# Performance work log

Hardware: AMD Instinct MI355X
Metric: run time of the kernel (lower is better)

## Reference

```python
import jax, jax.numpy as jnp
import numpy as np

ALPHA = 0.1   # alpha_factor
BETA = 1.0    # beta_factor
NUM_CLASSES = 1000
B, D = 4096, 512


def setup_inputs() -> dict:
    key = jax.random.key(0)
    ks = jax.random.split(key, 7)
    return {
        "anchor": jax.random.normal(ks[0], (B, D), dtype=jnp.float32),
        "positive": jax.random.normal(ks[1], (B, D), dtype=jnp.float32),
        "negative": jax.random.normal(ks[2], (B, D), dtype=jnp.float32),
        "outputs": jax.random.normal(ks[3], (3 * B, NUM_CLASSES), dtype=jnp.float32),
        "labels_anchor": jax.random.randint(ks[4], (B,), 0, NUM_CLASSES, dtype=jnp.int32).astype(jnp.int64),
        "labels_neg": jax.random.randint(ks[5], (B,), 0, NUM_CLASSES, dtype=jnp.int32).astype(jnp.int64),
        "exemplars": jax.random.normal(ks[6], (NUM_CLASSES, D), dtype=jnp.float32),
    }


def reference(anchor, positive, negative, outputs, labels_anchor, labels_neg, exemplars):
    # cross-entropy (mean reduction) over concatenated labels [3B]
    labels = jnp.concatenate([labels_anchor, labels_anchor, labels_neg], axis=0)
    logp = jax.nn.log_softmax(outputs, axis=-1)                       # [3B, C]
    loss_softmax = -jnp.mean(jnp.take_along_axis(logp, labels[:, None], axis=1))

    # pairwise L2 distances anchor-to-exemplars via ||a||^2 + ||e||^2 - 2 a.e  -> [B, C]
    a_sq = jnp.sum(anchor * anchor, axis=1, keepdims=True)            # [B, 1]
    e_sq = jnp.sum(exemplars * exemplars, axis=1)[None, :]            # [1, C]
    d2 = a_sq + e_sq - 2.0 * (anchor @ exemplars.T)                   # [B, C]
    d_all = jnp.sqrt(jnp.maximum(d2, 0.0))

    d_ref = jnp.take_along_axis(d_all, labels_anchor[:, None], axis=1)[:, 0]  # [B]
    d_closest = jnp.min(d_all, axis=1)                                # [B]
    loss_center = jnp.sum(jax.nn.relu(d_ref - d_closest))

    tp = jnp.linalg.norm(anchor - positive, axis=1)                   # [B]
    tn = jnp.linalg.norm(anchor - negative, axis=1)                   # [B]
    loss_triplet = jnp.sum(jax.nn.relu(tp - tn))

    loss_total = loss_softmax + ALPHA * loss_center + BETA * loss_triplet
    return (loss_total, loss_triplet, loss_softmax, loss_center)
```

## Files before the change

### kernel.cpp

```cpp
#include <hip/hip_runtime.h>
#include <math.h>

#define BB 4096
#define DD 512
#define CC 1000

typedef __attribute__((ext_vector_type(8))) short short8;
typedef __attribute__((ext_vector_type(4))) float f32x4;

#define OFF_PMINP 0
#define OFF_DREF  32768
#define OFF_CEP   36864
#define OFF_TRP   38400

__device__ __forceinline__ unsigned short f2bf(float x) {
    unsigned u = __float_as_uint(x);
    unsigned r = (u + 0x7FFFu + ((u >> 16) & 1u)) >> 16;
    return (unsigned short)r;
}

__device__ __forceinline__ short8 cvt8(const float4 x, const float4 y, float& sq) {
    union { unsigned short u[8]; short8 v; } o;
    o.u[0]=f2bf(x.x); o.u[1]=f2bf(x.y); o.u[2]=f2bf(x.z); o.u[3]=f2bf(x.w);
    o.u[4]=f2bf(y.x); o.u[5]=f2bf(y.y); o.u[6]=f2bf(y.z); o.u[7]=f2bf(y.w);
    sq += x.x*x.x + x.y*x.y + x.z*x.z + x.w*x.w
        + y.x*y.x + y.y*y.y + y.z*y.z + y.w*y.w;
    return o.v;
}

__global__ __launch_bounds__(512) void main_kernel(
    const float* __restrict__ a, const float* __restrict__ p,
    const float* __restrict__ n, const float* __restrict__ ex,
    const float* __restrict__ outp,
    const int* __restrict__ la, const int* __restrict__ ln,
    float* __restrict__ pminp, float* __restrict__ ce_part,
    float* __restrict__ tr_part, float* __restrict__ dref)
{
    __shared__ unsigned short lA[128 * 64];
    __shared__ unsigned short lB[128 * 64];
    __shared__ float s_pm[4][128];
    __shared__ float s_aq[128], s_eq[128];
    __shared__ float ps[8];

    const int bid = blockIdx.x;
    const int tid = threadIdx.x;
    const int w = tid >> 6, lane = tid & 63;

    if (bid < 256) {
        const int strip = bid & 31, panel = bid >> 5;
        const int gm0 = strip * 128, gn0 = panel * 128;
        const int wm = w >> 2, wn = w & 3;
        const int hi = lane >> 4, lo = lane & 15;

        const int r0 = tid >> 3, s0 = tid & 7;
        const int g0 = s0 ^ (r0 & 7);
        const float4* srcA0 = (const float4*)(a + (size_t)(gm0 + r0) * DD) + (g0 << 1);
        const float4* srcA1 = (const float4*)(a + (size_t)(gm0 + 64 + r0) * DD) + (g0 << 1);
        const int er0 = gn0 + r0,      er0c = er0 < CC ? er0 : CC - 1;
        const int er1 = gn0 + 64 + r0, er1c = er1 < CC ? er1 : CC - 1;
        const float4* srcB0 = (const float4*)(ex + (size_t)er0c * DD) + (g0 << 1);
        const float4* srcB1 = (const float4*)(ex + (size_t)er1c * DD) + (g0 << 1);

        float4 a0, a0b, a1, a1b, b0, b0b, b1, b1b;
#define GLOAD(kt) do { \
        a0 = srcA0[(kt)*16]; a0b = srcA0[(kt)*16 + 1]; \
        a1 = srcA1[(kt)*16]; a1b = srcA1[(kt)*16 + 1]; \
        b0 = srcB0[(kt)*16]; b0b = srcB0[(kt)*16 + 1]; \
        b1 = srcB1[(kt)*16]; b1b = srcB1[(kt)*16 + 1]; \
    } while (0)

        float sa0 = 0.f, sa1 = 0.f, se0 = 0.f, se1 = 0.f;
        f32x4 acc[4][2];
#pragma unroll
        for (int mi = 0; mi < 4; mi++)
#pragma unroll
            for (int ni = 0; ni < 2; ni++) acc[mi][ni] = (f32x4){0.f, 0.f, 0.f, 0.f};

        GLOAD(0);
        for (int kt = 0; kt < 8; kt++) {
            *(short8*)&lA[tid << 3]         = cvt8(a0, a0b, sa0);
            *(short8*)&lA[(tid + 512) << 3] = cvt8(a1, a1b, sa1);
            *(short8*)&lB[tid << 3]         = cvt8(b0, b0b, se0);
            *(short8*)&lB[(tid + 512) << 3] = cvt8(b1, b1b, se1);
            __syncthreads();
            if (kt < 7) GLOAD(kt + 1);

#pragma unroll
            for (int kk = 0; kk < 2; kk++) {
                short8 af[4], bf[2];
#pragma unroll
                for (int mi = 0; mi < 4; mi++) {
                    int r = (wm << 6) + (mi << 4) + lo, s = (kk << 2) + hi;
                    af[mi] = *(const short8*)&lA[(r << 6) + ((s ^ (r & 7)) << 3)];
                }
#pragma unroll
                for (int ni = 0; ni < 2; ni++) {
                    int r = (wn << 5) + (ni << 4) + lo, s = (kk << 2) + hi;
                    bf[ni] = *(const short8*)&lB[(r << 6) + ((s ^ (r & 7)) << 3)];
                }
#pragma unroll
                for (int mi = 0; mi < 4; mi++)
#pragma unroll
                    for (int ni = 0; ni < 2; ni++)
                        acc[mi][ni] = __builtin_amdgcn_mfma_f32_16x16x32_bf16(af[mi], bf[ni], acc[mi][ni], 0, 0, 0);
            }
            __syncthreads();
        }
#undef GLOAD

#pragma unroll
        for (int off = 1; off < 8; off <<= 1) {
            sa0 += __shfl_xor(sa0, off);
            sa1 += __shfl_xor(sa1, off);
            se0 += __shfl_xor(se0, off);
            se1 += __shfl_xor(se1, off);
        }
        if ((lane & 7) == 0) {
            s_aq[r0] = sa0; s_aq[64 + r0] = sa1;
            s_eq[r0] = se0; s_eq[64 + r0] = se1;
        }
        __syncthreads();

        float aq[4][4];
#pragma unroll
        for (int mi = 0; mi < 4; mi++)
#pragma unroll
            for (int j = 0; j < 4; j++)
                aq[mi][j] = s_aq[wm * 64 + mi * 16 + hi * 4 + j];
        float esqc[2]; int bad[2];
#pragma unroll
        for (int ni = 0; ni < 2; ni++) {
            int gn = gn0 + wn * 32 + ni * 16 + lo;
            esqc[ni] = s_eq[wn * 32 + ni * 16 + lo];
            bad[ni] = (gn >= CC);
        }
        float vmin[4][4];
#pragma unroll
        for (int mi = 0; mi < 4; mi++)
#pragma unroll
            for (int j = 0; j < 4; j++) {
                float best = INFINITY;
#pragma unroll
                for (int ni = 0; ni < 2; ni++) {
                    float d2 = aq[mi][j] + esqc[ni] - 2.f * acc[mi][ni][j];
                    float d = sqrtf(fmaxf(d2, 0.f));
                    if (bad[ni]) d = INFINITY;
                    best = fminf(best, d);
                }
                vmin[mi][j] = best;
            }
#pragma unroll
        for (int off = 1; off < 16; off <<= 1)
#pragma unroll
            for (int mi = 0; mi < 4; mi++)
#pragma unroll
                for (int j = 0; j < 4; j++)
                    vmin[mi][j] = fminf(vmin[mi][j], __shfl_xor(vmin[mi][j], off));

        if (lo == 0) {
#pragma unroll
            for (int mi = 0; mi < 4; mi++)
#pragma unroll
                for (int j = 0; j < 4; j++)
                    s_pm[wn][wm * 64 + mi * 16 + hi * 4 + j] = vmin[mi][j];
        }
        __syncthreads();
        if (tid < 128) {
            float m2 = fminf(fminf(s_pm[0][tid], s_pm[1][tid]),
                             fminf(s_pm[2][tid], s_pm[3][tid]));
            pminp[((size_t)(gm0 + tid) << 3) + panel] = m2;
        }
    } else if (bid < 1792) {
        const int cb = bid - 256;
        const int r = cb * 8 + w;
        const int label = (r < 2 * BB) ? la[r & (BB - 1)] : ln[r - 2 * BB];
        const float4* row4 = (const float4*)(outp + (size_t)r * CC);
        float4 v[4];
#pragma unroll
        for (int k = 0; k < 4; k++) {
            int j4 = lane + k * 64;
            v[k] = (j4 < 250) ? row4[j4]
                              : make_float4(-INFINITY, -INFINITY, -INFINITY, -INFINITY);
        }
        float m = -INFINITY;
#pragma unroll
        for (int k = 0; k < 4; k++)
            m = fmaxf(m, fmaxf(fmaxf(v[k].x, v[k].y), fmaxf(v[k].z, v[k].w)));
        for (int off = 32; off; off >>= 1) m = fmaxf(m, __shfl_xor(m, off));

        const int lj4 = label >> 2, lc = label & 3;
        float s = 0.f, lv = 0.f;
#pragma unroll
        for (int k = 0; k < 4; k++) {
            int j4 = lane + k * 64;
            s += __expf(v[k].x - m) + __expf(v[k].y - m)
               + __expf(v[k].z - m) + __expf(v[k].w - m);
            float comp = (lc == 0) ? v[k].x : (lc == 1) ? v[k].y : (lc == 2) ? v[k].z : v[k].w;
            lv += (j4 == lj4) ? comp : 0.f;
        }
        for (int off = 32; off; off >>= 1) {
            s += __shfl_xor(s, off);
            lv += __shfl_xor(lv, off);
        }
        if (lane == 0) ps[w] = -(lv - m - __logf(s));
        __syncthreads();
        if (tid == 0) {
            float t = 0.f;
#pragma unroll
            for (int q = 0; q < 8; q++) t += ps[q];
            ce_part[cb] = t;
        }
    } else {
        const int i = (bid - 1792) * 8 + w;
        const int label = la[i];
        const float4* ar = (const float4*)(a + (size_t)i * DD);
        const float4* pr = (const float4*)(p + (size_t)i * DD);
        const float4* nr = (const float4*)(n + (size_t)i * DD);
        const float4* er = (const float4*)(ex + (size_t)label * DD);
        float sp = 0.f, sn = 0.f, se = 0.f;
#pragma unroll
        for (int k = 0; k < 2; k++) {
            const int j = lane + k * 64;
            float4 av = ar[j], pv = pr[j], nv = nr[j], ev = er[j];
            float dx = av.x-pv.x, dy = av.y-pv.y, dz = av.z-pv.z, dw = av.w-pv.w;
            sp += dx*dx + dy*dy + dz*dz + dw*dw;
            dx = av.x-nv.x; dy = av.y-nv.y; dz = av.z-nv.z; dw = av.w-nv.w;
            sn += dx*dx + dy*dy + dz*dz + dw*dw;
            dx = av.x-ev.x; dy = av.y-ev.y; dz = av.z-ev.z; dw = av.w-ev.w;
            se += dx*dx + dy*dy + dz*dz + dw*dw;
        }
        for (int off = 32; off; off >>= 1) {
            sp += __shfl_xor(sp, off);
            sn += __shfl_xor(sn, off);
            se += __shfl_xor(se, off);
        }
        if (lane == 0) {
            dref[i] = sqrtf(se);
            ps[w] = fmaxf(sqrtf(sp) - sqrtf(sn), 0.f);
        }
        __syncthreads();
        if (tid == 0) {
            float t = 0.f;
#pragma unroll
            for (int q = 0; q < 8; q++) t += ps[q];
            tr_part[bid - 1792] = t;
        }
    }
}

__global__ __launch_bounds__(1024) void final_kernel(
    const float* __restrict__ ce_part, const float* __restrict__ tr_part,
    const float* __restrict__ pminp, const float* __restrict__ dref,
    float* __restrict__ out)
{
    int tid = threadIdx.x;
    float ce = ce_part[tid] + ((tid < 512) ? ce_part[tid + 1024] : 0.f);
    float tr = (tid < 512) ? tr_part[tid] : 0.f;
    float ctr = 0.f;
    float4 d4 = *(const float4*)&dref[tid * 4];
#pragma unroll
    for (int k = 0; k < 4; k++) {
        int m = tid * 4 + k;
        float4 p0 = *(const float4*)&pminp[(size_t)m * 8];
        float4 p1 = *(const float4*)&pminp[(size_t)m * 8 + 4];
        float mn = fminf(fminf(fminf(p0.x, p0.y), fminf(p0.z, p0.w)),
                         fminf(fminf(p1.x, p1.y), fminf(p1.z, p1.w)));
        float dr = (k == 0) ? d4.x : (k == 1) ? d4.y : (k == 2) ? d4.z : d4.w;
        ctr += fmaxf(dr - mn, 0.f);
    }
    for (int off = 32; off; off >>= 1) {
        ce += __shfl_xor(ce, off);
        tr += __shfl_xor(tr, off);
        ctr += __shfl_xor(ctr, off);
    }
    __shared__ float s[3][16];
    int wid = tid >> 6, lane = tid & 63;
    if (lane == 0) { s[0][wid] = ce; s[1][wid] = tr; s[2][wid] = ctr; }
    __syncthreads();
    if (tid == 0) {
        float tce = 0.f, ttr = 0.f, tctr = 0.f;
#pragma unroll
        for (int q = 0; q < 16; q++) { tce += s[0][q]; ttr += s[1][q]; tctr += s[2][q]; }
        float lsm = tce / (3.f * BB);
        out[0] = lsm + 0.1f * tctr + 1.0f * ttr;
        out[1] = ttr;
        out[2] = lsm;
        out[3] = tctr;
    }
}

extern "C" void kernel_launch(void* const* d_in, const int* in_sizes, int n_in,
                              void* d_out, int out_size, void* d_ws, size_t ws_size,
                              hipStream_t stream) {
    const float* anchor   = (const float*)d_in[0];
    const float* positive = (const float*)d_in[1];
    const float* negative = (const float*)d_in[2];
    const float* outputs  = (const float*)d_in[3];
    const int*   la       = (const int*)d_in[4];
    const int*   ln       = (const int*)d_in[5];
    const float* ex       = (const float*)d_in[6];
    float* out = (float*)d_out;
    float* ws  = (float*)d_ws;

    float* pminp    = ws + OFF_PMINP;
    float* dref     = ws + OFF_DREF;
    float* ce_part  = ws + OFF_CEP;
    float* tr_part  = ws + OFF_TRP;

    hipLaunchKernelGGL(main_kernel,  dim3(2304), dim3(512),  0, stream,
                       anchor, positive, negative, ex, outputs, la, ln,
                       pminp, ce_part, tr_part, dref);
    hipLaunchKernelGGL(final_kernel, dim3(1),    dim3(1024), 0, stream,
                       ce_part, tr_part, pminp, dref, out);
}
```

Measured before the change: 33.52 us.

## Halve GEMM strip height and interleave block roles across the grid

The distance-GEMM tile shrinks from 128x128 to 64x128 rows per block, which doubles the GEMM blocks to 512 and spreads them across more CUs. Block roles are interleaved with bid%5, so GEMM, cross-entropy and triplet blocks are mixed in the grid instead of being launched in contiguous ranges. Launch bounds now request 4 blocks per CU to raise occupancy. The cost is that the exemplar tile is loaded from global memory twice as often, and each wave does less MFMA work per LDS read.

```diff
diff --git a/kernel.cpp b/kernel.cpp
--- a/kernel.cpp
+++ b/kernel.cpp
@@ -28,7 +28,7 @@
     return o.v;
 }
 
-__global__ __launch_bounds__(512) void main_kernel(
+__global__ __launch_bounds__(512, 4) void main_kernel(
     const float* __restrict__ a, const float* __restrict__ p,
     const float* __restrict__ n, const float* __restrict__ ex,
     const float* __restrict__ outp,
@@ -36,50 +36,48 @@
     float* __restrict__ pminp, float* __restrict__ ce_part,
     float* __restrict__ tr_part, float* __restrict__ dref)
 {
-    __shared__ unsigned short lA[128 * 64];
+    __shared__ unsigned short lA[64 * 64];
     __shared__ unsigned short lB[128 * 64];
-    __shared__ float s_pm[4][128];
-    __shared__ float s_aq[128], s_eq[128];
+    __shared__ float s_pm[4][64];
+    __shared__ float s_aq[64], s_eq[128];
     __shared__ float ps[8];
 
     const int bid = blockIdx.x;
     const int tid = threadIdx.x;
     const int w = tid >> 6, lane = tid & 63;
-
-    if (bid < 256) {
-        const int strip = bid & 31, panel = bid >> 5;
-        const int gm0 = strip * 128, gn0 = panel * 128;
+    const int role = bid % 5, idx = bid / 5;
+
+    if (role == 0) {
+        const int strip = idx & 63, panel = idx >> 6;
+        const int gm0 = strip * 64, gn0 = panel * 128;
         const int wm = w >> 2, wn = w & 3;
         const int hi = lane >> 4, lo = lane & 15;
 
         const int r0 = tid >> 3, s0 = tid & 7;
         const int g0 = s0 ^ (r0 & 7);
         const float4* srcA0 = (const float4*)(a + (size_t)(gm0 + r0) * DD) + (g0 << 1);
-        const float4* srcA1 = (const float4*)(a + (size_t)(gm0 + 64 + r0) * DD) + (g0 << 1);
-        const int er0 = gn0 + r0,      er0c = er0 < CC ? er0 : CC - 1;
-        const int er1 = gn0 + 64 + r0, er1c = er1 < CC ? er1 : CC - 1;
-        const float4* srcB0 = (const float4*)(ex + (size_t)er0c * DD) + (g0 << 1);
-        const float4* srcB1 = (const float4*)(ex + (size_t)er1c * DD) + (g0 << 1);
-
-        float4 a0, a0b, a1, a1b, b0, b0b, b1, b1b;
+        int er0 = gn0 + r0;      er0 = er0 < CC ? er0 : CC - 1;
+        int er1 = gn0 + 64 + r0; er1 = er1 < CC ? er1 : CC - 1;
+        const float4* srcB0 = (const float4*)(ex + (size_t)er0 * DD) + (g0 << 1);
+        const float4* srcB1 = (const float4*)(ex + (size_t)er1 * DD) + (g0 << 1);
+
+        float4 a0, a0b, b0, b0b, b1, b1b;
 #define GLOAD(kt) do { \
         a0 = srcA0[(kt)*16]; a0b = srcA0[(kt)*16 + 1]; \
-        a1 = srcA1[(kt)*16]; a1b = srcA1[(kt)*16 + 1]; \
         b0 = srcB0[(kt)*16]; b0b = srcB0[(kt)*16 + 1]; \
         b1 = srcB1[(kt)*16]; b1b = srcB1[(kt)*16 + 1]; \
     } while (0)
 
-        float sa0 = 0.f, sa1 = 0.f, se0 = 0.f, se1 = 0.f;
-        f32x4 acc[4][2];
-#pragma unroll
-        for (int mi = 0; mi < 4; mi++)
+        float sa0 = 0.f, se0 = 0.f, se1 = 0.f;
+        f32x4 acc[2][2];
+#pragma unroll
+        for (int mi = 0; mi < 2; mi++)
 #pragma unroll
             for (int ni = 0; ni < 2; ni++) acc[mi][ni] = (f32x4){0.f, 0.f, 0.f, 0.f};
 
         GLOAD(0);
         for (int kt = 0; kt < 8; kt++) {
             *(short8*)&lA[tid << 3]         = cvt8(a0, a0b, sa0);
-            *(short8*)&lA[(tid + 512) << 3] = cvt8(a1, a1b, sa1);
             *(short8*)&lB[tid << 3]         = cvt8(b0, b0b, se0);
             *(short8*)&lB[(tid + 512) << 3] = cvt8(b1, b1b, se1);
             __syncthreads();
@@ -87,10 +85,10 @@
 
 #pragma unroll
             for (int kk = 0; kk < 2; kk++) {
-                short8 af[4], bf[2];
-#pragma unroll
-                for (int mi = 0; mi < 4; mi++) {
-                    int r = (wm << 6) + (mi << 4) + lo, s = (kk << 2) + hi;
+                short8 af[2], bf[2];
+#pragma unroll
+                for (int mi = 0; mi < 2; mi++) {
+                    int r = (wm << 5) + (mi << 4) + lo, s = (kk << 2) + hi;
                     af[mi] = *(const short8*)&lA[(r << 6) + ((s ^ (r & 7)) << 3)];
                 }
 #pragma unroll
@@ -99,7 +97,7 @@
                     bf[ni] = *(const short8*)&lB[(r << 6) + ((s ^ (r & 7)) << 3)];
                 }
 #pragma unroll
-                for (int mi = 0; mi < 4; mi++)
+                for (int mi = 0; mi < 2; mi++)
 #pragma unroll
                     for (int ni = 0; ni < 2; ni++)
                         acc[mi][ni] = __builtin_amdgcn_mfma_f32_16x16x32_bf16(af[mi], bf[ni], acc[mi][ni], 0, 0, 0);
@@ -111,22 +109,21 @@
 #pragma unroll
         for (int off = 1; off < 8; off <<= 1) {
             sa0 += __shfl_xor(sa0, off);
-            sa1 += __shfl_xor(sa1, off);
             se0 += __shfl_xor(se0, off);
             se1 += __shfl_xor(se1, off);
         }
-        if ((lane & 7) == 0) {
-            s_aq[r0] = sa0; s_aq[64 + r0] = sa1;
+        if (s0 == 0) {
+            s_aq[r0] = sa0;
             s_eq[r0] = se0; s_eq[64 + r0] = se1;
         }
         __syncthreads();
 
-        float aq[4][4];
-#pragma unroll
-        for (int mi = 0; mi < 4; mi++)
+        float aq[2][4];
+#pragma unroll
+        for (int mi = 0; mi < 2; mi++)
 #pragma unroll
             for (int j = 0; j < 4; j++)
-                aq[mi][j] = s_aq[wm * 64 + mi * 16 + hi * 4 + j];
+                aq[mi][j] = s_aq[wm * 32 + mi * 16 + hi * 4 + j];
         float esqc[2]; int bad[2];
 #pragma unroll
         for (int ni = 0; ni < 2; ni++) {
@@ -134,9 +131,9 @@
             esqc[ni] = s_eq[wn * 32 + ni * 16 + lo];
             bad[ni] = (gn >= CC);
         }
-        float vmin[4][4];
-#pragma unroll
-        for (int mi = 0; mi < 4; mi++)
+        float vmin[2][4];
+#pragma unroll
+        for (int mi = 0; mi < 2; mi++)
 #pragma unroll
             for (int j = 0; j < 4; j++) {
                 float best = INFINITY;
@@ -152,26 +149,26 @@
 #pragma unroll
         for (int off = 1; off < 16; off <<= 1)
 #pragma unroll
-            for (int mi = 0; mi < 4; mi++)
+            for (int mi = 0; mi < 2; mi++)
 #pragma unroll
                 for (int j = 0; j < 4; j++)
                     vmin[mi][j] = fminf(vmin[mi][j], __shfl_xor(vmin[mi][j], off));
 
         if (lo == 0) {
 #pragma unroll
-            for (int mi = 0; mi < 4; mi++)
+            for (int mi = 0; mi < 2; mi++)
 #pragma unroll
                 for (int j = 0; j < 4; j++)
-                    s_pm[wn][wm * 64 + mi * 16 + hi * 4 + j] = vmin[mi][j];
+                    s_pm[wn][wm * 32 + mi * 16 + hi * 4 + j] = vmin[mi][j];
         }
         __syncthreads();
-        if (tid < 128) {
+        if (tid < 64) {
             float m2 = fminf(fminf(s_pm[0][tid], s_pm[1][tid]),
                              fminf(s_pm[2][tid], s_pm[3][tid]));
             pminp[((size_t)(gm0 + tid) << 3) + panel] = m2;
         }
-    } else if (bid < 1792) {
-        const int cb = bid - 256;
+    } else if (role < 4) {
+        const int cb = idx * 3 + (role - 1);
         const int r = cb * 8 + w;
         const int label = (r < 2 * BB) ? la[r & (BB - 1)] : ln[r - 2 * BB];
         const float4* row4 = (const float4*)(outp + (size_t)r * CC);
@@ -211,7 +208,7 @@
             ce_part[cb] = t;
         }
     } else {
-        const int i = (bid - 1792) * 8 + w;
+        const int i = idx * 8 + w;
         const int label = la[i];
         const float4* ar = (const float4*)(a + (size_t)i * DD);
         const float4* pr = (const float4*)(p + (size_t)i * DD);
@@ -243,7 +240,7 @@
             float t = 0.f;
 #pragma unroll
             for (int q = 0; q < 8; q++) t += ps[q];
-            tr_part[bid - 1792] = t;
+            tr_part[idx] = t;
         }
     }
 }
@@ -307,7 +304,7 @@
     float* ce_part  = ws + OFF_CEP;
     float* tr_part  = ws + OFF_TRP;
 
-    hipLaunchKernelGGL(main_kernel,  dim3(2304), dim3(512),  0, stream,
+    hipLaunchKernelGGL(main_kernel,  dim3(2560), dim3(512),  0, stream,
                        anchor, positive, negative, ex, outputs, la, ln,
                        pminp, ce_part, tr_part, dref);
     hipLaunchKernelGGL(final_kernel, dim3(1),    dim3(1024), 0, stream,
```

Result: slower. 41.66 us (+24.3%).
